# Kernel optimization log

Measured on AMD Instinct MI355X. Metric: run time of the kernel, lower is better.

The kernel has to match this reference:

```python
import jax, jax.numpy as jnp
import numpy as np
import math

N_BINS = 100  # len(torch.arange(0.01, 1.01, 0.01))


def _soft_histogram_masks(H, W, dtype=jnp.float32):
    # radial distance from image center, 'ij' meshgrid like torch.meshgrid default
    a = jnp.arange(H, dtype=dtype)[:, None]   # rows
    b = jnp.arange(W, dtype=dtype)[None, :]   # cols
    dist = jnp.sqrt((a - H / 2) ** 2 + (b - W / 2) ** 2)  # [H, W]
    max_radius = math.sqrt(H * H + W * W) / 2
    radius_factors = jnp.arange(1, N_BINS + 1, dtype=dtype) * 0.01  # 0.01 .. 1.00
    radius_set = max_radius * radius_factors                        # [100]
    # s[i] = sigmoid(r_i - dist); bin mask i = s[i] - s[i-1], mask 0 = s[0]
    s = jax.nn.sigmoid(radius_set[:, None, None] - dist[None])      # [100, H, W]
    masks = s - jnp.concatenate([jnp.zeros((1, H, W), dtype), s[:-1]], axis=0)
    return masks  # [100, H, W]


def setup_inputs() -> dict:
    key = jax.random.key(0)
    k1, k2 = jax.random.split(key)
    B, C, H, W = 16, 3, 512, 512
    x = jax.random.normal(k1, (B, C, H, W), dtype=jnp.float32)
    value_set = jax.random.uniform(k2, (B, N_BINS), dtype=jnp.float32)
    return {"x": x, "value_set": value_set}


def reference(x, value_set):
    B, C, H, W = x.shape
    fq_mask_set = _soft_histogram_masks(H, W, x.dtype)           # [100, H, W]
    # weighted sum over bins; avoids materializing [B, 100, H, W]
    fq_mask = jnp.einsum('br,rhw->bhw', value_set, fq_mask_set)  # [B, H, W]
    return (fq_mask, value_set)
```

## Files before the change

### kernel.cpp

```cpp
#include <hip/hip_runtime.h>
#include <math.h>

#define HDIM   512
#define WDIM   512
#define BATCH  16
#define NBINS  100
#define NPIX   (HDIM * WDIM)

#define STEP      3.6203867196751236f
#define INV_STEP  0.27621358640099516f
#define CUT       13.0f

__global__ __launch_bounds__(256) void fq_mask_kernel(
    const float* __restrict__ value_set,
    float* __restrict__ out_mask,
    float* __restrict__ out_vs)
{
    __shared__ float vs[BATCH * NBINS];
    const int tid = threadIdx.x;
    #pragma unroll
    for (int i = tid; i < BATCH * NBINS; i += 256) vs[i] = value_set[i];
    __syncthreads();

    const int pix = blockIdx.x * 256 + tid;
    const int h = pix >> 9;
    const int w = pix & (WDIM - 1);

    const float dy = (float)h - (float)(HDIM / 2);
    const float dx = (float)w - (float)(WDIM / 2);
    const float dist = sqrtf(dy * dy + dx * dx);

    int r_lo = (int)floorf((dist - CUT) * INV_STEP);
    if (r_lo < 0) r_lo = 0;
    int r_hi = (int)floorf((dist + CUT) * INV_STEP);
    if (r_hi > NBINS - 1) r_hi = NBINS - 1;

    float acc[BATCH];
    #pragma unroll
    for (int b = 0; b < BATCH; ++b) acc[b] = 0.0f;

    float s_prev = 0.0f;
    for (int r = r_lo; r <= r_hi; ++r) {
        float xr = STEP * (float)(r + 1) - dist;
        float e  = __expf(-xr);
        float s  = __fdividef(1.0f, 1.0f + e);
        float m  = s - s_prev;
        s_prev = s;
        #pragma unroll
        for (int b = 0; b < BATCH; ++b)
            acc[b] = fmaf(vs[b * NBINS + r], m, acc[b]);
    }

    #pragma unroll
    for (int b = 0; b < BATCH; ++b)
        out_mask[b * NPIX + pix] = acc[b];

    if (blockIdx.x == 0) {
        #pragma unroll
        for (int i = tid; i < BATCH * NBINS; i += 256) out_vs[i] = vs[i];
    }
}

extern "C" void kernel_launch(void* const* d_in, const int* in_sizes, int n_in,
                              void* d_out, int out_size, void* d_ws, size_t ws_size,
                              hipStream_t stream) {
    const float* value_set = (const float*)d_in[1];
    float* out_mask = (float*)d_out;
    float* out_vs   = (float*)d_out + BATCH * NPIX;

    const int threads = 256;
    const int blocks  = NPIX / threads;
    fq_mask_kernel<<<blocks, threads, 0, stream>>>(value_set, out_mask, out_vs);
}
```

Measured before the change: 12.01 us.

## Process four pixels per thread in 32x32 tiles with transposed bin weights

Each thread now computes four adjacent pixels inside a 32x32 tile, so every float4 shared-memory load of the transposed value table is reused across four pixels. The sigmoid is evaluated with a geometric exp recurrence and a hardware reciprocal instead of an exp per bin, and the output is written with float4 stores. The bin cutoff window is narrowed from 13 to 8 pixels, which drops more of the sigmoid tails and may loosen accuracy. The grid shrinks to 256 blocks, which lowers the number of waves available for occupancy.

```diff
diff --git a/kernel.cpp b/kernel.cpp
--- a/kernel.cpp
+++ b/kernel.cpp
@@ -9,55 +9,96 @@
 
 #define STEP      3.6203867196751236f
 #define INV_STEP  0.27621358640099516f
-#define CUT       13.0f
+#define CUT       8.0f
+#define VSTRIDE   20
+
+__device__ __forceinline__ float4 fma4(float a, float4 m, float4 c) {
+    c.x = fmaf(a, m.x, c.x);
+    c.y = fmaf(a, m.y, c.y);
+    c.z = fmaf(a, m.z, c.z);
+    c.w = fmaf(a, m.w, c.w);
+    return c;
+}
 
 __global__ __launch_bounds__(256) void fq_mask_kernel(
     const float* __restrict__ value_set,
     float* __restrict__ out_mask,
     float* __restrict__ out_vs)
 {
-    __shared__ float vs[BATCH * NBINS];
+    __shared__ __align__(16) float vst[NBINS * VSTRIDE];
     const int tid = threadIdx.x;
-    #pragma unroll
-    for (int i = tid; i < BATCH * NBINS; i += 256) vs[i] = value_set[i];
+    for (int i = tid; i < BATCH * NBINS; i += 256) {
+        int b = i / NBINS;
+        int r = i - b * NBINS;
+        vst[r * VSTRIDE + b] = value_set[i];
+    }
     __syncthreads();
 
-    const int pix = blockIdx.x * 256 + tid;
-    const int h = pix >> 9;
-    const int w = pix & (WDIM - 1);
+    const int lane   = tid & 63;
+    const int wv     = tid >> 6;
+    const int row_in = wv * 8 + (lane >> 3);
+    const int col_in = (lane & 7) * 4;
+    const int by = blockIdx.x >> 4;
+    const int bx = blockIdx.x & 15;
+    const int h  = by * 32 + row_in;
+    const int w  = bx * 32 + col_in;
 
-    const float dy = (float)h - (float)(HDIM / 2);
-    const float dx = (float)w - (float)(WDIM / 2);
-    const float dist = sqrtf(dy * dy + dx * dx);
+    const float fy  = (float)h - 256.0f;
+    const float dy2 = fy * fy;
+    float d[4];
+    #pragma unroll
+    for (int p = 0; p < 4; ++p) {
+        float dx = (float)(w + p) - 256.0f;
+        d[p] = sqrtf(dy2 + dx * dx);
+    }
+    const float dmin = fminf(fminf(d[0], d[1]), fminf(d[2], d[3]));
+    const float dmax = fmaxf(fmaxf(d[0], d[1]), fmaxf(d[2], d[3]));
+    int r_lo = (int)floorf((dmin - CUT) * INV_STEP); if (r_lo < 0) r_lo = 0;
+    int r_hi = (int)floorf((dmax + CUT) * INV_STEP); if (r_hi > NBINS - 1) r_hi = NBINS - 1;
+    const int cnt = r_hi - r_lo + 1;
 
-    int r_lo = (int)floorf((dist - CUT) * INV_STEP);
-    if (r_lo < 0) r_lo = 0;
-    int r_hi = (int)floorf((dist + CUT) * INV_STEP);
-    if (r_hi > NBINS - 1) r_hi = NBINS - 1;
-
-    float acc[BATCH];
+    const float dec = __expf(-STEP);
+    float e[4], sp[4];
     #pragma unroll
-    for (int b = 0; b < BATCH; ++b) acc[b] = 0.0f;
-
-    float s_prev = 0.0f;
-    for (int r = r_lo; r <= r_hi; ++r) {
-        float xr = STEP * (float)(r + 1) - dist;
-        float e  = __expf(-xr);
-        float s  = __fdividef(1.0f, 1.0f + e);
-        float m  = s - s_prev;
-        s_prev = s;
-        #pragma unroll
-        for (int b = 0; b < BATCH; ++b)
-            acc[b] = fmaf(vs[b * NBINS + r], m, acc[b]);
+    for (int p = 0; p < 4; ++p) {
+        e[p]  = __expf(d[p] - STEP * (float)(r_lo + 1));
+        sp[p] = 0.0f;
     }
 
+    float4 acc[BATCH];
+    #pragma unroll
+    for (int b = 0; b < BATCH; ++b) acc[b] = make_float4(0.f, 0.f, 0.f, 0.f);
+
+    int r = r_lo;
+    for (int i = 0; i < cnt; ++i, ++r) {
+        float mm[4];
+        #pragma unroll
+        for (int p = 0; p < 4; ++p) {
+            float s = __builtin_amdgcn_rcpf(1.0f + e[p]);
+            mm[p]  = s - sp[p];
+            sp[p]  = s;
+            e[p]  *= dec;
+        }
+        const float4 m = make_float4(mm[0], mm[1], mm[2], mm[3]);
+        const float4* vr = (const float4*)&vst[r * VSTRIDE];
+        #pragma unroll
+        for (int c = 0; c < 4; ++c) {
+            float4 v = vr[c];
+            acc[4*c + 0] = fma4(v.x, m, acc[4*c + 0]);
+            acc[4*c + 1] = fma4(v.y, m, acc[4*c + 1]);
+            acc[4*c + 2] = fma4(v.z, m, acc[4*c + 2]);
+            acc[4*c + 3] = fma4(v.w, m, acc[4*c + 3]);
+        }
+    }
+
+    const int pixbase = h * WDIM + w;
     #pragma unroll
     for (int b = 0; b < BATCH; ++b)
-        out_mask[b * NPIX + pix] = acc[b];
+        *(float4*)&out_mask[b * NPIX + pixbase] = acc[b];
 
     if (blockIdx.x == 0) {
-        #pragma unroll
-        for (int i = tid; i < BATCH * NBINS; i += 256) out_vs[i] = vs[i];
+        for (int i = tid; i < BATCH * NBINS; i += 256)
+            out_vs[i] = value_set[i];
     }
 }
 
@@ -69,6 +110,6 @@
     float* out_vs   = (float*)d_out + BATCH * NPIX;
 
     const int threads = 256;
-    const int blocks  = NPIX / threads;
+    const int blocks  = (HDIM / 32) * (WDIM / 32);
     fq_mask_kernel<<<blocks, threads, 0, stream>>>(value_set, out_mask, out_vs);
 }
```

Measured after the change: 11.81 us. About the same (-1.7%).
